# Optimization experiments

Hardware: AMD Instinct MI355X
Metric: run time of the kernel (lower is better)

The kernel has to match this reference:

```python
import jax, jax.numpy as jnp
import numpy as np

NUM_USERS = 50000
NUM_MOVIES = 20000
NNZ = 2000000
NUM_POS = NNZ // 10
NEG_SAMPLE_SIZE = 5
IN_FEATS = 128
NUM_HIDDEN = 64
BETA = 0.01
GAMMA = 0.01


def setup_inputs() -> dict:
    key = jax.random.key(0)
    ks = jax.random.split(key, 10)
    features = jax.random.normal(ks[0], (NUM_MOVIES, IN_FEATS), dtype=jnp.float32)
    W_enc = jax.random.normal(ks[1], (IN_FEATS, NUM_HIDDEN), dtype=jnp.float32) / np.sqrt(IN_FEATS)
    b_enc = jnp.zeros((NUM_HIDDEN,), dtype=jnp.float32)
    W_p = jax.random.normal(ks[2], (NUM_HIDDEN, NUM_HIDDEN), dtype=jnp.float32) / np.sqrt(NUM_HIDDEN)
    W_q = jax.random.normal(ks[3], (NUM_HIDDEN, NUM_HIDDEN), dtype=jnp.float32) / np.sqrt(NUM_HIDDEN)
    b_u = jnp.zeros((NUM_USERS,), dtype=jnp.float32)
    b_i = jnp.zeros((NUM_MOVIES,), dtype=jnp.float32)
    vals = jax.random.uniform(ks[4], (NNZ,), dtype=jnp.float32) + 0.5  # positive ratings
    rows = jax.random.randint(ks[5], (NNZ,), 0, NUM_USERS, dtype=jnp.int32)
    cols = jax.random.randint(ks[6], (NNZ,), 0, NUM_MOVIES, dtype=jnp.int32)
    pos_idx = jax.random.randint(ks[7], (NUM_POS,), 0, NNZ, dtype=jnp.int32)
    neg_item_idx = jax.random.randint(ks[8], (NUM_POS * NEG_SAMPLE_SIZE,), 0, NUM_MOVIES, dtype=jnp.int32)
    return {
        "features": features, "W_enc": W_enc, "b_enc": b_enc,
        "W_p": W_p, "W_q": W_q, "b_u": b_u, "b_i": b_i,
        "vals": vals, "rows": rows, "cols": cols,
        "pos_idx": pos_idx, "neg_item_idx": neg_item_idx,
        "neg_sample_size": NEG_SAMPLE_SIZE,
    }


def reference(features, W_enc, b_enc, W_p, W_q, b_u, b_i,
              vals, rows, cols, pos_idx, neg_item_idx, neg_sample_size):
    # encode + gconv projections -> item factor matrices P, Q  [M, d]
    h = features @ W_enc + b_enc
    P = h @ W_p
    Q = h @ W_q

    # sparse COO matmul: user_emb_full[u] = sum_{(u,i) in spm} vals * P[i]
    user_emb_full = jax.ops.segment_sum(vals[:, None] * P[cols], rows,
                                        num_segments=NUM_USERS)  # [U, d]
    # user_deg = spm.dot(ones)
    user_deg = jax.ops.segment_sum(vals, rows, num_segments=NUM_USERS)  # [U]

    def est_rating(user_idx, item_idx):
        bu = b_u[user_idx]
        bi = b_i[item_idx]
        ue = user_emb_full[user_idx] / user_deg[user_idx][:, None]
        return bu + bi + jnp.sum(ue * Q[item_idx], axis=1)

    user_idx = rows[pos_idx]
    item_idx = cols[pos_idx]
    r_ui = est_rating(user_idx, item_idx)[:, None]                 # [P, 1]
    neg_user_idx = jnp.repeat(user_idx, neg_sample_size)
    neg_r_ui = est_rating(neg_user_idx, neg_item_idx).reshape(-1, neg_sample_size)  # [P, S]

    diff = 1.0 - (r_ui - neg_r_ui)
    loss = (jnp.sum(diff * diff) * 0.5
            + BETA * 0.5 * jnp.sum(P * P + Q * Q)
            + GAMMA * 0.5 * (jnp.sum(b_u * b_u) + jnp.sum(b_i * b_i)))
    return loss
```

## Files before the change

### kernel.cpp

```cpp
#include <hip/hip_runtime.h>

#define HIDDEN 64
#define BETA 0.01f
#define GAMMA 0.01f

#define BUCKET_SHIFT 8
#define BUCKET_W     (1 << BUCKET_SHIFT)
#define TILE_E       8192

__device__ inline unsigned short f2bf(float f) {
    unsigned x = __float_as_uint(f);
    return (unsigned short)((x + 0x7fffu + ((x >> 16) & 1u)) >> 16);
}
__device__ inline float bf2f(unsigned short b) {
    return __uint_as_float(((unsigned)b) << 16);
}
__device__ inline float bflo(unsigned w) { return __uint_as_float(w << 16); }
__device__ inline float bfhi(unsigned w) {
    return __uint_as_float(w & 0xffff0000u);
}

__global__ void __launch_bounds__(256)
encode_kernel(const float* __restrict__ features,
              const float* __restrict__ W_enc,
              const float* __restrict__ b_enc,
              const float* __restrict__ W_p,
              const float* __restrict__ W_q,
              unsigned short* __restrict__ Ph,
              unsigned short* __restrict__ Qh,
              float* __restrict__ partials, int slot_base,
              int num_movies, int in_feats) {
    __shared__ float hs[16][HIDDEN];
    const int tid = threadIdx.x;
    const int j = tid & 63;
    const int wv = tid >> 6;
    const int m0 = blockIdx.x * 16 + wv * 4;

    const int c0 = min(m0 + 0, num_movies - 1);
    const int c1 = min(m0 + 1, num_movies - 1);
    const int c2 = min(m0 + 2, num_movies - 1);
    const int c3 = min(m0 + 3, num_movies - 1);
    const float* fr0 = features + (size_t)c0 * in_feats;
    const float* fr1 = features + (size_t)c1 * in_feats;
    const float* fr2 = features + (size_t)c2 * in_feats;
    const float* fr3 = features + (size_t)c3 * in_feats;

    float h0 = 0.0f, h1 = 0.0f, h2 = 0.0f, h3 = 0.0f;
    #pragma unroll 4
    for (int f = 0; f < in_feats; f += 4) {
        const float w_a = W_enc[(f + 0) * HIDDEN + j];
        const float w_b = W_enc[(f + 1) * HIDDEN + j];
        const float w_c = W_enc[(f + 2) * HIDDEN + j];
        const float w_d = W_enc[(f + 3) * HIDDEN + j];
        const float4 a0 = *(const float4*)(fr0 + f);
        const float4 a1 = *(const float4*)(fr1 + f);
        const float4 a2 = *(const float4*)(fr2 + f);
        const float4 a3 = *(const float4*)(fr3 + f);
        h0 = fmaf(a0.x, w_a, h0); h0 = fmaf(a0.y, w_b, h0);
        h0 = fmaf(a0.z, w_c, h0); h0 = fmaf(a0.w, w_d, h0);
        h1 = fmaf(a1.x, w_a, h1); h1 = fmaf(a1.y, w_b, h1);
        h1 = fmaf(a1.z, w_c, h1); h1 = fmaf(a1.w, w_d, h1);
        h2 = fmaf(a2.x, w_a, h2); h2 = fmaf(a2.y, w_b, h2);
        h2 = fmaf(a2.z, w_c, h2); h2 = fmaf(a2.w, w_d, h2);
        h3 = fmaf(a3.x, w_a, h3); h3 = fmaf(a3.y, w_b, h3);
        h3 = fmaf(a3.z, w_c, h3); h3 = fmaf(a3.w, w_d, h3);
    }
    const float be = b_enc[j];
    hs[wv * 4 + 0][j] = h0 + be;
    hs[wv * 4 + 1][j] = h1 + be;
    hs[wv * 4 + 2][j] = h2 + be;
    hs[wv * 4 + 3][j] = h3 + be;
    __syncthreads();

    float p0 = 0.0f, p1 = 0.0f, p2 = 0.0f, p3 = 0.0f;
    float q0 = 0.0f, q1 = 0.0f, q2 = 0.0f, q3 = 0.0f;
    #pragma unroll 4
    for (int f = 0; f < HIDDEN; f += 4) {
        const float wp0 = W_p[(f + 0) * HIDDEN + j];
        const float wp1 = W_p[(f + 1) * HIDDEN + j];
        const float wp2 = W_p[(f + 2) * HIDDEN + j];
        const float wp3 = W_p[(f + 3) * HIDDEN + j];
        const float wq0 = W_q[(f + 0) * HIDDEN + j];
        const float wq1 = W_q[(f + 1) * HIDDEN + j];
        const float wq2 = W_q[(f + 2) * HIDDEN + j];
        const float wq3 = W_q[(f + 3) * HIDDEN + j];
        const float4 v0 = *(const float4*)(&hs[wv * 4 + 0][f]);
        const float4 v1 = *(const float4*)(&hs[wv * 4 + 1][f]);
        const float4 v2 = *(const float4*)(&hs[wv * 4 + 2][f]);
        const float4 v3 = *(const float4*)(&hs[wv * 4 + 3][f]);
        p0 = fmaf(v0.x, wp0, p0); p0 = fmaf(v0.y, wp1, p0);
        p0 = fmaf(v0.z, wp2, p0); p0 = fmaf(v0.w, wp3, p0);
        q0 = fmaf(v0.x, wq0, q0); q0 = fmaf(v0.y, wq1, q0);
        q0 = fmaf(v0.z, wq2, q0); q0 = fmaf(v0.w, wq3, q0);
        p1 = fmaf(v1.x, wp0, p1); p1 = fmaf(v1.y, wp1, p1);
        p1 = fmaf(v1.z, wp2, p1); p1 = fmaf(v1.w, wp3, p1);
        q1 = fmaf(v1.x, wq0, q1); q1 = fmaf(v1.y, wq1, q1);
        q1 = fmaf(v1.z, wq2, q1); q1 = fmaf(v1.w, wq3, q1);
        p2 = fmaf(v2.x, wp0, p2); p2 = fmaf(v2.y, wp1, p2);
        p2 = fmaf(v2.z, wp2, p2); p2 = fmaf(v2.w, wp3, p2);
        q2 = fmaf(v2.x, wq0, q2); q2 = fmaf(v2.y, wq1, q2);
        q2 = fmaf(v2.z, wq2, q2); q2 = fmaf(v2.w, wq3, q2);
        p3 = fmaf(v3.x, wp0, p3); p3 = fmaf(v3.y, wp1, p3);
        p3 = fmaf(v3.z, wp2, p3); p3 = fmaf(v3.w, wp3, p3);
        q3 = fmaf(v3.x, wq0, q3); q3 = fmaf(v3.y, wq1, q3);
        q3 = fmaf(v3.z, wq2, q3); q3 = fmaf(v3.w, wq3, q3);
    }

    float reg = 0.0f;
    if (m0 + 0 < num_movies) {
        Ph[(size_t)(m0 + 0) * HIDDEN + j] = f2bf(p0);
        Qh[(size_t)(m0 + 0) * HIDDEN + j] = f2bf(q0);
        reg += p0 * p0 + q0 * q0;
    }
    if (m0 + 1 < num_movies) {
        Ph[(size_t)(m0 + 1) * HIDDEN + j] = f2bf(p1);
        Qh[(size_t)(m0 + 1) * HIDDEN + j] = f2bf(q1);
        reg += p1 * p1 + q1 * q1;
    }
    if (m0 + 2 < num_movies) {
        Ph[(size_t)(m0 + 2) * HIDDEN + j] = f2bf(p2);
        Qh[(size_t)(m0 + 2) * HIDDEN + j] = f2bf(q2);
        reg += p2 * p2 + q2 * q2;
    }
    if (m0 + 3 < num_movies) {
        Ph[(size_t)(m0 + 3) * HIDDEN + j] = f2bf(p3);
        Qh[(size_t)(m0 + 3) * HIDDEN + j] = f2bf(q3);
        reg += p3 * p3 + q3 * q3;
    }

    for (int off = 32; off; off >>= 1) reg += __shfl_down(reg, off);
    __shared__ float s_part[4];
    if (j == 0) s_part[wv] = reg;
    __syncthreads();
    if (tid == 0) {
        float t = (s_part[0] + s_part[1]) + (s_part[2] + s_part[3]);
        partials[slot_base + blockIdx.x] = 0.5f * BETA * t;
    }
}

__global__ void tilehist_kernel(const int* __restrict__ rows, int nnz,
                                int nbuckets, int ntiles,
                                unsigned* __restrict__ tileHist) {
    extern __shared__ unsigned hist[];
    const int t = blockIdx.x;
    const int tid = threadIdx.x;
    for (int i = tid; i < nbuckets; i += blockDim.x) hist[i] = 0;
    __syncthreads();

    const int base = t * TILE_E;
    const int kmax = TILE_E / 256;
    for (int k = 0; k < kmax; ++k) {
        const int e = base + k * 256 + tid;
        if (e < nnz) {
            const int r = __builtin_nontemporal_load(rows + e);
            atomicAdd(&hist[r >> BUCKET_SHIFT], 1u);
        }
    }
    __syncthreads();
    for (int i = tid; i < nbuckets; i += blockDim.x)
        tileHist[(size_t)i * ntiles + t] = hist[i];
}

__global__ void chunksum_kernel(const unsigned* __restrict__ src, int n,
                                unsigned* __restrict__ sums) {
    __shared__ unsigned s[256];
    const int t = threadIdx.x;
    const int i = blockIdx.x * 256 + t;
    s[t] = (i < n) ? src[i] : 0u;
    __syncthreads();
    for (int off = 128; off; off >>= 1) {
        if (t < off) s[t] += s[t + off];
        __syncthreads();
    }
    if (t == 0) sums[blockIdx.x] = s[0];
}

__global__ void __launch_bounds__(512)
scantop_kernel(const unsigned* __restrict__ sums, int nchunks,
               unsigned* __restrict__ chunk_off,
               unsigned* __restrict__ offs, int n, int total) {
    __shared__ unsigned s[512];
    const int t = threadIdx.x;
    unsigned x = (t < nchunks) ? sums[t] : 0u;
    s[t] = x;
    __syncthreads();
    for (int off = 1; off < 512; off <<= 1) {
        unsigned v = (t >= off) ? s[t - off] : 0u;
        __syncthreads();
        s[t] += v;
        __syncthreads();
    }
    if (t < nchunks) chunk_off[t] = s[t] - x;
    if (t == 0) offs[n] = (unsigned)total;
}

__global__ void exscan_kernel(const unsigned* __restrict__ src, int n,
                              const unsigned* __restrict__ chunk_off,
                              unsigned* __restrict__ dst) {
    __shared__ unsigned s[256];
    const int t = threadIdx.x;
    const int i = blockIdx.x * 256 + t;
    unsigned x = (i < n) ? src[i] : 0u;
    s[t] = x;
    __syncthreads();
    for (int off = 1; off < 256; off <<= 1) {
        unsigned v = (t >= off) ? s[t - off] : 0u;
        __syncthreads();
        s[t] += v;
        __syncthreads();
    }
    if (i < n) dst[i] = chunk_off[blockIdx.x] + s[t] - x;
}

__global__ void partition_kernel(const int* __restrict__ rows,
                                 const int* __restrict__ cols,
                                 const float* __restrict__ vals, int nnz,
                                 int nbuckets, int ntiles,
                                 const unsigned* __restrict__ offsB,
                                 uint2* __restrict__ temp) {
    extern __shared__ unsigned smem[];
    unsigned* hist = smem;
    unsigned* lofs = smem + nbuckets;
    const int t = blockIdx.x;
    const int tid = threadIdx.x;
    for (int i = tid; i < nbuckets; i += blockDim.x) {
        hist[i] = 0;
        lofs[i] = offsB[(size_t)i * ntiles + t];
    }
    __syncthreads();

    const int base = t * TILE_E;
    const int kmax = TILE_E / 256;
    for (int k = 0; k < kmax; ++k) {
        const int e = base + k * 256 + tid;
        if (e < nnz) {
            const int r = __builtin_nontemporal_load(rows + e);
            const int c = __builtin_nontemporal_load(cols + e);
            const float v = __builtin_nontemporal_load(vals + e);
            const int b = r >> BUCKET_SHIFT;
            const unsigned lrank = atomicAdd(&hist[b], 1u);
            const unsigned dst = lofs[b] + lrank;
            const unsigned key = ((unsigned)r << 15) | (unsigned)c;
            temp[dst] = make_uint2(key, __float_as_uint(v));
        }
    }
}

__global__ void __launch_bounds__(1024)
csr_scatter_kernel(const uint2* __restrict__ temp,
                   const unsigned* __restrict__ offsB,
                   int* __restrict__ row_start,
                   uint2* __restrict__ pairs,
                   int ntiles, int num_users, int nbB) {
    __shared__ int cnt[BUCKET_W];
    __shared__ int scan_s[BUCKET_W];
    __shared__ int cur[BUCKET_W];
    const int b = blockIdx.x;
    const int tid = threadIdx.x;
    const int ubase = b << BUCKET_SHIFT;
    const int s0 = (int)offsB[(size_t)b * ntiles];
    const int s1 = (int)offsB[(size_t)(b + 1) * ntiles];

    if (tid < BUCKET_W) cnt[tid] = 0;
    __syncthreads();
    const unsigned* tx = (const unsigned*)temp;
    for (int s = s0 + tid; s < s1; s += 1024) {
        const unsigned key = __builtin_nontemporal_load(tx + 2 * (size_t)s);
        atomicAdd(&cnt[(int)(key >> 15) - ubase], 1);
    }
    __syncthreads();

    int x = 0;
    if (tid < BUCKET_W) {
        x = cnt[tid];
        scan_s[tid] = x;
    }
    __syncthreads();
    for (int off = 1; off < BUCKET_W; off <<= 1) {
        int v = 0;
        if (tid < BUCKET_W && tid >= off) v = scan_s[tid - off];
        __syncthreads();
        if (tid < BUCKET_W) scan_s[tid] += v;
        __syncthreads();
    }
    if (tid < BUCKET_W) {
        const int start = s0 + scan_s[tid] - x;
        cur[tid] = start;
        if (ubase + tid < num_users) row_start[ubase + tid] = start;
    }
    if (b == nbB - 1 && tid == 0) row_start[num_users] = s1;
    __syncthreads();

    for (int s = s0 + tid; s < s1; s += 1024) {
        const unsigned long long ev = __builtin_nontemporal_load(
            (const unsigned long long*)temp + s);
        const unsigned ex = (unsigned)ev;
        const unsigned ey = (unsigned)(ev >> 32);
        const int lu = (int)(ex >> 15) - ubase;
        const int dst = atomicAdd(&cur[lu], 1);
        pairs[dst] = make_uint2(ex & 0x7fffu, ey);
    }
}

__global__ void gather_kernel(const int* __restrict__ row_start,
                              const uint2* __restrict__ pairs,
                              const unsigned short* __restrict__ Ph,
                              float* __restrict__ user_emb,
                              float* __restrict__ user_deg, int nu) {
    const int lane = threadIdx.x & 63;
    const int q  = lane >> 4;
    const int ql = lane & 15;
    const int u = (blockIdx.x * blockDim.x + threadIdx.x) >> 6;
    if (u >= nu) return;

    const int s0 = row_start[u];
    const int s1 = row_start[u + 1];
    float a0 = 0.0f, a1 = 0.0f, a2 = 0.0f, a3 = 0.0f, degA = 0.0f;
    float b0 = 0.0f, b1 = 0.0f, b2 = 0.0f, b3 = 0.0f, degB = 0.0f;
    int s = s0;
    for (; s + 7 < s1; s += 8) {
        const uint2 pA = pairs[s + q];
        const uint2 pB = pairs[s + 4 + q];
        const uint2 wA = *(const uint2*)(Ph + (size_t)pA.x * HIDDEN + 4 * ql);
        const uint2 wB = *(const uint2*)(Ph + (size_t)pB.x * HIDDEN + 4 * ql);
        const float vA = __uint_as_float(pA.y);
        const float vB = __uint_as_float(pB.y);
        a0 = fmaf(vA, bflo(wA.x), a0);
        a1 = fmaf(vA, bfhi(wA.x), a1);
        a2 = fmaf(vA, bflo(wA.y), a2);
        a3 = fmaf(vA, bfhi(wA.y), a3);
        b0 = fmaf(vB, bflo(wB.x), b0);
        b1 = fmaf(vB, bfhi(wB.x), b1);
        b2 = fmaf(vB, bflo(wB.y), b2);
        b3 = fmaf(vB, bfhi(wB.y), b3);
        degA += vA;
        degB += vB;
    }
    for (; s + 3 < s1; s += 4) {
        const uint2 pA = pairs[s + q];
        const uint2 wA = *(const uint2*)(Ph + (size_t)pA.x * HIDDEN + 4 * ql);
        const float vA = __uint_as_float(pA.y);
        a0 = fmaf(vA, bflo(wA.x), a0);
        a1 = fmaf(vA, bfhi(wA.x), a1);
        a2 = fmaf(vA, bflo(wA.y), a2);
        a3 = fmaf(vA, bfhi(wA.y), a3);
        degA += vA;
    }
    if (s + q < s1) {
        const uint2 pA = pairs[s + q];
        const uint2 wA = *(const uint2*)(Ph + (size_t)pA.x * HIDDEN + 4 * ql);
        const float vA = __uint_as_float(pA.y);
        a0 = fmaf(vA, bflo(wA.x), a0);
        a1 = fmaf(vA, bfhi(wA.x), a1);
        a2 = fmaf(vA, bflo(wA.y), a2);
        a3 = fmaf(vA, bfhi(wA.y), a3);
        degA += vA;
    }

    float x0 = a0 + b0, x1 = a1 + b1, x2 = a2 + b2, x3 = a3 + b3;
    float deg = degA + degB;
    x0 += __shfl_xor(x0, 16); x0 += __shfl_xor(x0, 32);
    x1 += __shfl_xor(x1, 16); x1 += __shfl_xor(x1, 32);
    x2 += __shfl_xor(x2, 16); x2 += __shfl_xor(x2, 32);
    x3 += __shfl_xor(x3, 16); x3 += __shfl_xor(x3, 32);
    deg += __shfl_xor(deg, 16); deg += __shfl_xor(deg, 32);
    if (q == 0) {
        *(float4*)(user_emb + (size_t)u * HIDDEN + 4 * ql) =
            make_float4(x0, x1, x2, x3);
        if (ql == 0) user_deg[u] = deg;
    }
}

__device__ inline float dot16(const uint4* __restrict__ q,
                              const float* __restrict__ ue) {
    float d = 0.0f;
    #pragma unroll
    for (int h = 0; h < 2; ++h) {
        const uint4 v = q[h];
        const unsigned w0 = v.x, w1 = v.y, w2 = v.z, w3 = v.w;
        d = fmaf(ue[h * 8 + 0], bflo(w0), d);
        d = fmaf(ue[h * 8 + 1], bfhi(w0), d);
        d = fmaf(ue[h * 8 + 2], bflo(w1), d);
        d = fmaf(ue[h * 8 + 3], bfhi(w1), d);
        d = fmaf(ue[h * 8 + 4], bflo(w2), d);
        d = fmaf(ue[h * 8 + 5], bfhi(w2), d);
        d = fmaf(ue[h * 8 + 6], bflo(w3), d);
        d = fmaf(ue[h * 8 + 7], bfhi(w3), d);
    }
    return d;
}

template <int S>
__global__ void loss4_kernel(const float* __restrict__ user_emb,
                             const float* __restrict__ user_deg,
                             const unsigned short* __restrict__ Qh,
                             const float* __restrict__ b_u,
                             const float* __restrict__ b_i,
                             const int* __restrict__ rows,
                             const int* __restrict__ cols,
                             const int* __restrict__ pos_idx,
                             const int* __restrict__ neg_item_idx,
                             int num_pos,
                             float* __restrict__ partials, int slot_base) {
    const int tid = blockIdx.x * blockDim.x + threadIdx.x;
    const int g = tid >> 2;
    const int l = tid & 3;
    float acc = 0.0f;

    if (g < num_pos) {
        const int e = pos_idx[g];
        const int u = rows[e];
        const int ii = cols[e];
        const float invdeg = 1.0f / user_deg[u];

        float ue[16];
        {
            const float4* uep =
                (const float4*)(user_emb + (size_t)u * HIDDEN + l * 16);
            #pragma unroll
            for (int k = 0; k < 4; ++k) {
                const float4 t4 = uep[k];
                ue[4 * k + 0] = t4.x * invdeg;
                ue[4 * k + 1] = t4.y * invdeg;
                ue[4 * k + 2] = t4.z * invdeg;
                ue[4 * k + 3] = t4.w * invdeg;
            }
        }

        int jarr[S];
        float part[1 + S];
        part[0] = dot16((const uint4*)(Qh + (size_t)ii * HIDDEN + l * 16), ue);
        #pragma unroll
        for (int s = 0; s < S; ++s) {
            const int j = neg_item_idx[(size_t)g * S + s];
            jarr[s] = j;
            part[1 + s] =
                dot16((const uint4*)(Qh + (size_t)j * HIDDEN + l * 16), ue);
        }

        #pragma unroll
        for (int k = 0; k < 1 + S; ++k) {
            part[k] += __shfl_xor(part[k], 1);
            part[k] += __shfl_xor(part[k], 2);
        }

        if (l == 0) {
            const float bu = b_u[u];
            const float r = bu + b_i[ii] + part[0];
            #pragma unroll
            for (int s = 0; s < S; ++s) {
                const float nr = bu + b_i[jarr[s]] + part[1 + s];
                const float diff = 1.0f - (r - nr);
                acc += 0.5f * diff * diff;
            }
        }
    }

    for (int off = 32; off; off >>= 1) acc += __shfl_down(acc, off);
    __shared__ float s_part[16];
    const int wave = threadIdx.x >> 6;
    const int lane = threadIdx.x & 63;
    if (lane == 0) s_part[wave] = acc;
    __syncthreads();
    if (threadIdx.x == 0) {
        float t = 0.0f;
        const int nw = blockDim.x >> 6;
        for (int w = 0; w < nw; ++w) t += s_part[w];
        partials[slot_base + blockIdx.x] = t;
    }
}

__global__ void loss_generic_kernel(const float* __restrict__ user_emb,
                                    const float* __restrict__ user_deg,
                                    const unsigned short* __restrict__ Qh,
                                    const float* __restrict__ b_u,
                                    const float* __restrict__ b_i,
                                    const int* __restrict__ rows,
                                    const int* __restrict__ cols,
                                    const int* __restrict__ pos_idx,
                                    const int* __restrict__ neg_item_idx,
                                    int num_pos, int S,
                                    float* __restrict__ partials,
                                    int slot_base) {
    const int p = blockIdx.x * blockDim.x + threadIdx.x;
    float acc = 0.0f;
    if (p < num_pos) {
        const int e = pos_idx[p];
        const int u = rows[e];
        const int ii = cols[e];
        const float invdeg = 1.0f / user_deg[u];
        float ue[HIDDEN];
        #pragma unroll
        for (int kk = 0; kk < HIDDEN; ++kk)
            ue[kk] = user_emb[(size_t)u * HIDDEN + kk] * invdeg;
        const float bu = b_u[u];
        float dot = 0.0f;
        #pragma unroll
        for (int kk = 0; kk < HIDDEN; ++kk)
            dot = fmaf(ue[kk], bf2f(Qh[(size_t)ii * HIDDEN + kk]), dot);
        const float rr = bu + b_i[ii] + dot;
        for (int s = 0; s < S; ++s) {
            const int j = neg_item_idx[(size_t)p * S + s];
            float dn = 0.0f;
            #pragma unroll
            for (int kk = 0; kk < HIDDEN; ++kk)
                dn = fmaf(ue[kk], bf2f(Qh[(size_t)j * HIDDEN + kk]), dn);
            const float nr = bu + b_i[j] + dn;
            const float diff = 1.0f - (rr - nr);
            acc += 0.5f * diff * diff;
        }
    }
    for (int off = 32; off; off >>= 1) acc += __shfl_down(acc, off);
    __shared__ float s_part[16];
    const int wave = threadIdx.x >> 6;
    const int lane = threadIdx.x & 63;
    if (lane == 0) s_part[wave] = acc;
    __syncthreads();
    if (threadIdx.x == 0) {
        float t = 0.0f;
        const int nw = blockDim.x >> 6;
        for (int w = 0; w < nw; ++w) t += s_part[w];
        partials[slot_base + blockIdx.x] = t;
    }
}

__global__ void __launch_bounds__(1024)
final_reduce_kernel(const float* __restrict__ partials, int n,
                    const float* __restrict__ b_u, int nu,
                    const float* __restrict__ b_i, int ni,
                    float* __restrict__ out) {
    __shared__ float s[1024];
    const int t = threadIdx.x;
    float a = 0.0f;
    for (int i = t; i < n; i += 1024) a += partials[i];
    float r = 0.0f;
    for (int i = t; i < nu; i += 1024) {
        const float v = b_u[i];
        r = fmaf(v, v, r);
    }
    for (int i = t; i < ni; i += 1024) {
        const float v = b_i[i];
        r = fmaf(v, v, r);
    }
    s[t] = a + 0.5f * GAMMA * r;
    __syncthreads();
    for (int off = 512; off; off >>= 1) {
        if (t < off) s[t] += s[t + off];
        __syncthreads();
    }
    if (t == 0) out[0] = s[0];
}

extern "C" void kernel_launch(void* const* d_in, const int* in_sizes, int n_in,
                              void* d_out, int out_size, void* d_ws, size_t ws_size,
                              hipStream_t stream) {
    const float* features     = (const float*)d_in[0];
    const float* W_enc        = (const float*)d_in[1];
    const float* b_enc        = (const float*)d_in[2];
    const float* W_p          = (const float*)d_in[3];
    const float* W_q          = (const float*)d_in[4];
    const float* b_u          = (const float*)d_in[5];
    const float* b_i          = (const float*)d_in[6];
    const float* vals         = (const float*)d_in[7];
    const int*   rows         = (const int*)d_in[8];
    const int*   cols         = (const int*)d_in[9];
    const int*   pos_idx      = (const int*)d_in[10];
    const int*   neg_item_idx = (const int*)d_in[11];

    const int num_users  = in_sizes[5];
    const int num_movies = in_sizes[6];
    const int in_feats   = in_sizes[0] / num_movies;
    const int nnz        = in_sizes[7];
    const int num_pos    = in_sizes[10];
    const int S          = in_sizes[11] / num_pos;

    const int nbB    = (num_users + BUCKET_W - 1) >> BUCKET_SHIFT;
    const int ntiles = (nnz + TILE_E - 1) / TILE_E;
    const int scanNB = nbB * ntiles;
    const int n1b    = (scanNB + 255) / 256;

    const int enc_blocks  = (num_movies + 15) / 16;
    const int loss_blocks = (S == 5) ? (int)(((size_t)num_pos * 4 + 255) / 256)
                                     : (num_pos + 255) / 256;
    const int slot_pq   = 0;
    const int slot_loss = enc_blocks;
    const int n_slots   = enc_blocks + loss_blocks;

    auto align256 = [](size_t x) { return (x + 255) & ~(size_t)255; };
    char* ws = (char*)d_ws;
    size_t off = 0;
    unsigned short* Ph = (unsigned short*)(ws + off);
    off += align256((size_t)num_movies * HIDDEN * 2);
    unsigned short* Qh = (unsigned short*)(ws + off);
    off += align256((size_t)num_movies * HIDDEN * 2);
    char* U = ws + off;
    const size_t emb_bytes = align256((size_t)num_users * HIDDEN * 4);
    const size_t tmp_bytes = align256((size_t)nnz * 8);
    uint2* temp     = (uint2*)U;
    float* user_emb = (float*)U;
    off += (emb_bytes > tmp_bytes) ? emb_bytes : tmp_bytes;
    float* user_deg = (float*)(ws + off); off += align256((size_t)num_users * 4);
    int*   row_start= (int*)(ws + off);   off += align256((size_t)(num_users + 1) * 4);
    unsigned* tileHistB = (unsigned*)(ws + off); off += align256((size_t)scanNB * 4);
    unsigned* offsB     = (unsigned*)(ws + off); off += align256((size_t)(scanNB + 1) * 4);
    unsigned* sums_b    = (unsigned*)(ws + off); off += align256(512 * 4);
    unsigned* top_b     = (unsigned*)(ws + off); off += align256(512 * 4);
    uint2* pairs        = (uint2*)(ws + off);    off += align256((size_t)nnz * 8);
    float* partials     = (float*)(ws + off);    off += align256((size_t)n_slots * 4);

    float* out = (float*)d_out;

    encode_kernel<<<enc_blocks, 256, 0, stream>>>(
        features, W_enc, b_enc, W_p, W_q, Ph, Qh, partials, slot_pq,
        num_movies, in_feats);

    tilehist_kernel<<<ntiles, 256, (size_t)nbB * 4, stream>>>(
        rows, nnz, nbB, ntiles, tileHistB);
    chunksum_kernel<<<n1b, 256, 0, stream>>>(tileHistB, scanNB, sums_b);
    scantop_kernel<<<1, 512, 0, stream>>>(sums_b, n1b, top_b, offsB, scanNB, nnz);
    exscan_kernel<<<n1b, 256, 0, stream>>>(tileHistB, scanNB, top_b, offsB);

    partition_kernel<<<ntiles, 256, (size_t)nbB * 8, stream>>>(
        rows, cols, vals, nnz, nbB, ntiles, offsB, temp);
    csr_scatter_kernel<<<nbB, 1024, 0, stream>>>(temp, offsB, row_start,
                                                 pairs, ntiles, num_users, nbB);

    gather_kernel<<<(num_users * 64 + 255) / 256, 256, 0, stream>>>(
        row_start, pairs, Ph, user_emb, user_deg, num_users);

    if (S == 5) {
        loss4_kernel<5><<<loss_blocks, 256, 0, stream>>>(
            user_emb, user_deg, Qh, b_u, b_i, rows, cols, pos_idx,
            neg_item_idx, num_pos, partials, slot_loss);
    } else {
        loss_generic_kernel<<<loss_blocks, 256, 0, stream>>>(
            user_emb, user_deg, Qh, b_u, b_i, rows, cols, pos_idx,
            neg_item_idx, num_pos, S, partials, slot_loss);
    }

    final_reduce_kernel<<<1, 1024, 0, stream>>>(partials, n_slots,
                                                b_u, num_users,
                                                b_i, num_movies, out);
}
```

Measured before the change: 180.7 us.

## Compute per-user row offsets via global histogram scan; prefetch pairs in gather

Per-user counts are now accumulated with global atomics during the tile histogram pass, then scanned with the existing chunksum/scantop/exscan kernels to produce row_start. This removes the in-bucket count pass and shared-memory scan from csr_scatter. The gather loop is software-pipelined so the next pair loads are issued before the current Ph loads, and index loads use nontemporal hints. In exchange it adds 2M global atomics on a 50K-entry array, a memset, and three extra small kernel launches.

```diff
diff --git a/kernel.cpp b/kernel.cpp
--- a/kernel.cpp
+++ b/kernel.cpp
@@ -140,7 +140,8 @@
 
 __global__ void tilehist_kernel(const int* __restrict__ rows, int nnz,
                                 int nbuckets, int ntiles,
-                                unsigned* __restrict__ tileHist) {
+                                unsigned* __restrict__ tileHist,
+                                int* __restrict__ counts_u) {
     extern __shared__ unsigned hist[];
     const int t = blockIdx.x;
     const int tid = threadIdx.x;
@@ -154,6 +155,7 @@
         if (e < nnz) {
             const int r = __builtin_nontemporal_load(rows + e);
             atomicAdd(&hist[r >> BUCKET_SHIFT], 1u);
+            atomicAdd(&counts_u[r], 1);
         }
     }
     __syncthreads();
@@ -249,11 +251,9 @@
 __global__ void __launch_bounds__(1024)
 csr_scatter_kernel(const uint2* __restrict__ temp,
                    const unsigned* __restrict__ offsB,
-                   int* __restrict__ row_start,
+                   const int* __restrict__ row_start,
                    uint2* __restrict__ pairs,
-                   int ntiles, int num_users, int nbB) {
-    __shared__ int cnt[BUCKET_W];
-    __shared__ int scan_s[BUCKET_W];
+                   int ntiles, int num_users) {
     __shared__ int cur[BUCKET_W];
     const int b = blockIdx.x;
     const int tid = threadIdx.x;
@@ -261,34 +261,10 @@
     const int s0 = (int)offsB[(size_t)b * ntiles];
     const int s1 = (int)offsB[(size_t)(b + 1) * ntiles];
 
-    if (tid < BUCKET_W) cnt[tid] = 0;
-    __syncthreads();
-    const unsigned* tx = (const unsigned*)temp;
-    for (int s = s0 + tid; s < s1; s += 1024) {
-        const unsigned key = __builtin_nontemporal_load(tx + 2 * (size_t)s);
-        atomicAdd(&cnt[(int)(key >> 15) - ubase], 1);
-    }
-    __syncthreads();
-
-    int x = 0;
     if (tid < BUCKET_W) {
-        x = cnt[tid];
-        scan_s[tid] = x;
-    }
-    __syncthreads();
-    for (int off = 1; off < BUCKET_W; off <<= 1) {
-        int v = 0;
-        if (tid < BUCKET_W && tid >= off) v = scan_s[tid - off];
-        __syncthreads();
-        if (tid < BUCKET_W) scan_s[tid] += v;
-        __syncthreads();
-    }
-    if (tid < BUCKET_W) {
-        const int start = s0 + scan_s[tid] - x;
-        cur[tid] = start;
-        if (ubase + tid < num_users) row_start[ubase + tid] = start;
-    }
-    if (b == nbB - 1 && tid == 0) row_start[num_users] = s1;
+        const int gu = ubase + tid;
+        cur[tid] = (gu < num_users) ? row_start[gu] : 0;
+    }
     __syncthreads();
 
     for (int s = s0 + tid; s < s1; s += 1024) {
@@ -300,6 +276,12 @@
         const int dst = atomicAdd(&cur[lu], 1);
         pairs[dst] = make_uint2(ex & 0x7fffu, ey);
     }
+}
+
+__device__ inline uint2 ldnt2(const uint2* p) {
+    const unsigned long long v =
+        __builtin_nontemporal_load((const unsigned long long*)p);
+    return make_uint2((unsigned)v, (unsigned)(v >> 32));
 }
 
 __global__ void gather_kernel(const int* __restrict__ row_start,
@@ -317,27 +299,54 @@
     const int s1 = row_start[u + 1];
     float a0 = 0.0f, a1 = 0.0f, a2 = 0.0f, a3 = 0.0f, degA = 0.0f;
     float b0 = 0.0f, b1 = 0.0f, b2 = 0.0f, b3 = 0.0f, degB = 0.0f;
+
+    const int n8 = (s1 - s0) >> 3;
     int s = s0;
-    for (; s + 7 < s1; s += 8) {
-        const uint2 pA = pairs[s + q];
-        const uint2 pB = pairs[s + 4 + q];
-        const uint2 wA = *(const uint2*)(Ph + (size_t)pA.x * HIDDEN + 4 * ql);
-        const uint2 wB = *(const uint2*)(Ph + (size_t)pB.x * HIDDEN + 4 * ql);
-        const float vA = __uint_as_float(pA.y);
-        const float vB = __uint_as_float(pB.y);
-        a0 = fmaf(vA, bflo(wA.x), a0);
-        a1 = fmaf(vA, bfhi(wA.x), a1);
-        a2 = fmaf(vA, bflo(wA.y), a2);
-        a3 = fmaf(vA, bfhi(wA.y), a3);
-        b0 = fmaf(vB, bflo(wB.x), b0);
-        b1 = fmaf(vB, bfhi(wB.x), b1);
-        b2 = fmaf(vB, bflo(wB.y), b2);
-        b3 = fmaf(vB, bfhi(wB.y), b3);
-        degA += vA;
-        degB += vB;
-    }
-    for (; s + 3 < s1; s += 4) {
-        const uint2 pA = pairs[s + q];
+    if (n8 > 0) {
+        uint2 pA = ldnt2(pairs + s + q);
+        uint2 pB = ldnt2(pairs + s + 4 + q);
+        for (int it = 1; it < n8; ++it) {
+            const int sn = s + 8;
+            const uint2 nA = ldnt2(pairs + sn + q);
+            const uint2 nB = ldnt2(pairs + sn + 4 + q);
+            const uint2 wA = *(const uint2*)(Ph + (size_t)pA.x * HIDDEN + 4 * ql);
+            const uint2 wB = *(const uint2*)(Ph + (size_t)pB.x * HIDDEN + 4 * ql);
+            const float vA = __uint_as_float(pA.y);
+            const float vB = __uint_as_float(pB.y);
+            a0 = fmaf(vA, bflo(wA.x), a0);
+            a1 = fmaf(vA, bfhi(wA.x), a1);
+            a2 = fmaf(vA, bflo(wA.y), a2);
+            a3 = fmaf(vA, bfhi(wA.y), a3);
+            b0 = fmaf(vB, bflo(wB.x), b0);
+            b1 = fmaf(vB, bfhi(wB.x), b1);
+            b2 = fmaf(vB, bflo(wB.y), b2);
+            b3 = fmaf(vB, bfhi(wB.y), b3);
+            degA += vA;
+            degB += vB;
+            pA = nA;
+            pB = nB;
+            s = sn;
+        }
+        {
+            const uint2 wA = *(const uint2*)(Ph + (size_t)pA.x * HIDDEN + 4 * ql);
+            const uint2 wB = *(const uint2*)(Ph + (size_t)pB.x * HIDDEN + 4 * ql);
+            const float vA = __uint_as_float(pA.y);
+            const float vB = __uint_as_float(pB.y);
+            a0 = fmaf(vA, bflo(wA.x), a0);
+            a1 = fmaf(vA, bfhi(wA.x), a1);
+            a2 = fmaf(vA, bflo(wA.y), a2);
+            a3 = fmaf(vA, bfhi(wA.y), a3);
+            b0 = fmaf(vB, bflo(wB.x), b0);
+            b1 = fmaf(vB, bfhi(wB.x), b1);
+            b2 = fmaf(vB, bflo(wB.y), b2);
+            b3 = fmaf(vB, bfhi(wB.y), b3);
+            degA += vA;
+            degB += vB;
+            s += 8;
+        }
+    }
+    if (s + 3 < s1) {
+        const uint2 pA = ldnt2(pairs + s + q);
         const uint2 wA = *(const uint2*)(Ph + (size_t)pA.x * HIDDEN + 4 * ql);
         const float vA = __uint_as_float(pA.y);
         a0 = fmaf(vA, bflo(wA.x), a0);
@@ -345,9 +354,10 @@
         a2 = fmaf(vA, bflo(wA.y), a2);
         a3 = fmaf(vA, bfhi(wA.y), a3);
         degA += vA;
+        s += 4;
     }
     if (s + q < s1) {
-        const uint2 pA = pairs[s + q];
+        const uint2 pA = ldnt2(pairs + s + q);
         const uint2 wA = *(const uint2*)(Ph + (size_t)pA.x * HIDDEN + 4 * ql);
         const float vA = __uint_as_float(pA.y);
         a0 = fmaf(vA, bflo(wA.x), a0);
@@ -408,7 +418,7 @@
     float acc = 0.0f;
 
     if (g < num_pos) {
-        const int e = pos_idx[g];
+        const int e = __builtin_nontemporal_load(pos_idx + g);
         const int u = rows[e];
         const int ii = cols[e];
         const float invdeg = 1.0f / user_deg[u];
@@ -432,7 +442,8 @@
         part[0] = dot16((const uint4*)(Qh + (size_t)ii * HIDDEN + l * 16), ue);
         #pragma unroll
         for (int s = 0; s < S; ++s) {
-            const int j = neg_item_idx[(size_t)g * S + s];
+            const int j = __builtin_nontemporal_load(
+                neg_item_idx + (size_t)g * S + s);
             jarr[s] = j;
             part[1 + s] =
                 dot16((const uint4*)(Qh + (size_t)j * HIDDEN + l * 16), ue);
@@ -578,6 +589,7 @@
     const int ntiles = (nnz + TILE_E - 1) / TILE_E;
     const int scanNB = nbB * ntiles;
     const int n1b    = (scanNB + 255) / 256;
+    const int n1u    = (num_users + 255) / 256;
 
     const int enc_blocks  = (num_movies + 15) / 16;
     const int loss_blocks = (S == 5) ? (int)(((size_t)num_pos * 4 + 255) / 256)
@@ -600,30 +612,42 @@
     float* user_emb = (float*)U;
     off += (emb_bytes > tmp_bytes) ? emb_bytes : tmp_bytes;
     float* user_deg = (float*)(ws + off); off += align256((size_t)num_users * 4);
+    int*   counts_u = (int*)(ws + off);   off += align256((size_t)num_users * 4);
     int*   row_start= (int*)(ws + off);   off += align256((size_t)(num_users + 1) * 4);
     unsigned* tileHistB = (unsigned*)(ws + off); off += align256((size_t)scanNB * 4);
     unsigned* offsB     = (unsigned*)(ws + off); off += align256((size_t)(scanNB + 1) * 4);
     unsigned* sums_b    = (unsigned*)(ws + off); off += align256(512 * 4);
     unsigned* top_b     = (unsigned*)(ws + off); off += align256(512 * 4);
+    unsigned* sums_u    = (unsigned*)(ws + off); off += align256(512 * 4);
+    unsigned* top_u     = (unsigned*)(ws + off); off += align256(512 * 4);
     uint2* pairs        = (uint2*)(ws + off);    off += align256((size_t)nnz * 8);
     float* partials     = (float*)(ws + off);    off += align256((size_t)n_slots * 4);
 
     float* out = (float*)d_out;
+
+    hipMemsetAsync(counts_u, 0, (size_t)num_users * 4, stream);
 
     encode_kernel<<<enc_blocks, 256, 0, stream>>>(
         features, W_enc, b_enc, W_p, W_q, Ph, Qh, partials, slot_pq,
         num_movies, in_feats);
 
     tilehist_kernel<<<ntiles, 256, (size_t)nbB * 4, stream>>>(
-        rows, nnz, nbB, ntiles, tileHistB);
+        rows, nnz, nbB, ntiles, tileHistB, counts_u);
     chunksum_kernel<<<n1b, 256, 0, stream>>>(tileHistB, scanNB, sums_b);
     scantop_kernel<<<1, 512, 0, stream>>>(sums_b, n1b, top_b, offsB, scanNB, nnz);
     exscan_kernel<<<n1b, 256, 0, stream>>>(tileHistB, scanNB, top_b, offsB);
 
+    chunksum_kernel<<<n1u, 256, 0, stream>>>((const unsigned*)counts_u,
+                                             num_users, sums_u);
+    scantop_kernel<<<1, 512, 0, stream>>>(sums_u, n1u, top_u,
+                                          (unsigned*)row_start, num_users, nnz);
+    exscan_kernel<<<n1u, 256, 0, stream>>>((const unsigned*)counts_u, num_users,
+                                           top_u, (unsigned*)row_start);
+
     partition_kernel<<<ntiles, 256, (size_t)nbB * 8, stream>>>(
         rows, cols, vals, nnz, nbB, ntiles, offsB, temp);
     csr_scatter_kernel<<<nbB, 1024, 0, stream>>>(temp, offsB, row_start,
-                                                 pairs, ntiles, num_users, nbB);
+                                                 pairs, ntiles, num_users);
 
     gather_kernel<<<(num_users * 64 + 255) / 256, 256, 0, stream>>>(
         row_start, pairs, Ph, user_emb, user_deg, num_users);
```

Result: slower. 266.9 us (+47.7%).

## Fuse CSR scatter and gather into one kernel using LDS-sorted buckets

Applied to the files above, without the earlier changes.

Merges the per-bucket CSR scatter and the per-user gather into a single kernel. Each 128-user bucket sorts its edges by user in shared memory (in chunks of up to 6144 edges) and then gathers and accumulates P rows straight from that buffer, so the global pairs array and row_start are no longer written and read back. It halves the bucket width so each block does less work, and handles overflow chunks with a read-modify-write into user_emb. The cost is fewer, larger blocks whose gather phase runs only 8 waves per block, which may expose more memory latency than the old one-wave-per-user launch.

```diff
diff --git a/kernel.cpp b/kernel.cpp
--- a/kernel.cpp
+++ b/kernel.cpp
@@ -4,9 +4,10 @@
 #define BETA 0.01f
 #define GAMMA 0.01f
 
-#define BUCKET_SHIFT 8
+#define BUCKET_SHIFT 7
 #define BUCKET_W     (1 << BUCKET_SHIFT)
 #define TILE_E       8192
+#define CAP          6144
 
 __device__ inline unsigned short f2bf(float f) {
     unsigned x = __float_as_uint(f);
@@ -246,129 +247,142 @@
     }
 }
 
-__global__ void __launch_bounds__(1024)
-csr_scatter_kernel(const uint2* __restrict__ temp,
-                   const unsigned* __restrict__ offsB,
-                   int* __restrict__ row_start,
-                   uint2* __restrict__ pairs,
-                   int ntiles, int num_users, int nbB) {
+__global__ void __launch_bounds__(512)
+scatter_gather_kernel(const uint2* __restrict__ temp,
+                      const unsigned* __restrict__ offsB,
+                      const unsigned short* __restrict__ Ph,
+                      float* __restrict__ user_emb,
+                      float* __restrict__ user_deg,
+                      int ntiles, int num_users) {
+    __shared__ uint2 ebuf[CAP];
     __shared__ int cnt[BUCKET_W];
-    __shared__ int scan_s[BUCKET_W];
+    __shared__ int lstart[BUCKET_W];
     __shared__ int cur[BUCKET_W];
+
     const int b = blockIdx.x;
     const int tid = threadIdx.x;
     const int ubase = b << BUCKET_SHIFT;
     const int s0 = (int)offsB[(size_t)b * ntiles];
     const int s1 = (int)offsB[(size_t)(b + 1) * ntiles];
 
-    if (tid < BUCKET_W) cnt[tid] = 0;
-    __syncthreads();
-    const unsigned* tx = (const unsigned*)temp;
-    for (int s = s0 + tid; s < s1; s += 1024) {
-        const unsigned key = __builtin_nontemporal_load(tx + 2 * (size_t)s);
-        atomicAdd(&cnt[(int)(key >> 15) - ubase], 1);
-    }
-    __syncthreads();
-
-    int x = 0;
-    if (tid < BUCKET_W) {
-        x = cnt[tid];
-        scan_s[tid] = x;
-    }
-    __syncthreads();
-    for (int off = 1; off < BUCKET_W; off <<= 1) {
-        int v = 0;
-        if (tid < BUCKET_W && tid >= off) v = scan_s[tid - off];
-        __syncthreads();
-        if (tid < BUCKET_W) scan_s[tid] += v;
-        __syncthreads();
-    }
-    if (tid < BUCKET_W) {
-        const int start = s0 + scan_s[tid] - x;
-        cur[tid] = start;
-        if (ubase + tid < num_users) row_start[ubase + tid] = start;
-    }
-    if (b == nbB - 1 && tid == 0) row_start[num_users] = s1;
-    __syncthreads();
-
-    for (int s = s0 + tid; s < s1; s += 1024) {
-        const unsigned long long ev = __builtin_nontemporal_load(
-            (const unsigned long long*)temp + s);
-        const unsigned ex = (unsigned)ev;
-        const unsigned ey = (unsigned)(ev >> 32);
-        const int lu = (int)(ex >> 15) - ubase;
-        const int dst = atomicAdd(&cur[lu], 1);
-        pairs[dst] = make_uint2(ex & 0x7fffu, ey);
-    }
-}
-
-__global__ void gather_kernel(const int* __restrict__ row_start,
-                              const uint2* __restrict__ pairs,
-                              const unsigned short* __restrict__ Ph,
-                              float* __restrict__ user_emb,
-                              float* __restrict__ user_deg, int nu) {
-    const int lane = threadIdx.x & 63;
-    const int q  = lane >> 4;
+    const int wv = tid >> 6;
+    const int lane = tid & 63;
+    const int q = lane >> 4;
     const int ql = lane & 15;
-    const int u = (blockIdx.x * blockDim.x + threadIdx.x) >> 6;
-    if (u >= nu) return;
-
-    const int s0 = row_start[u];
-    const int s1 = row_start[u + 1];
-    float a0 = 0.0f, a1 = 0.0f, a2 = 0.0f, a3 = 0.0f, degA = 0.0f;
-    float b0 = 0.0f, b1 = 0.0f, b2 = 0.0f, b3 = 0.0f, degB = 0.0f;
-    int s = s0;
-    for (; s + 7 < s1; s += 8) {
-        const uint2 pA = pairs[s + q];
-        const uint2 pB = pairs[s + 4 + q];
-        const uint2 wA = *(const uint2*)(Ph + (size_t)pA.x * HIDDEN + 4 * ql);
-        const uint2 wB = *(const uint2*)(Ph + (size_t)pB.x * HIDDEN + 4 * ql);
-        const float vA = __uint_as_float(pA.y);
-        const float vB = __uint_as_float(pB.y);
-        a0 = fmaf(vA, bflo(wA.x), a0);
-        a1 = fmaf(vA, bfhi(wA.x), a1);
-        a2 = fmaf(vA, bflo(wA.y), a2);
-        a3 = fmaf(vA, bfhi(wA.y), a3);
-        b0 = fmaf(vB, bflo(wB.x), b0);
-        b1 = fmaf(vB, bfhi(wB.x), b1);
-        b2 = fmaf(vB, bflo(wB.y), b2);
-        b3 = fmaf(vB, bfhi(wB.y), b3);
-        degA += vA;
-        degB += vB;
-    }
-    for (; s + 3 < s1; s += 4) {
-        const uint2 pA = pairs[s + q];
-        const uint2 wA = *(const uint2*)(Ph + (size_t)pA.x * HIDDEN + 4 * ql);
-        const float vA = __uint_as_float(pA.y);
-        a0 = fmaf(vA, bflo(wA.x), a0);
-        a1 = fmaf(vA, bfhi(wA.x), a1);
-        a2 = fmaf(vA, bflo(wA.y), a2);
-        a3 = fmaf(vA, bfhi(wA.y), a3);
-        degA += vA;
-    }
-    if (s + q < s1) {
-        const uint2 pA = pairs[s + q];
-        const uint2 wA = *(const uint2*)(Ph + (size_t)pA.x * HIDDEN + 4 * ql);
-        const float vA = __uint_as_float(pA.y);
-        a0 = fmaf(vA, bflo(wA.x), a0);
-        a1 = fmaf(vA, bfhi(wA.x), a1);
-        a2 = fmaf(vA, bflo(wA.y), a2);
-        a3 = fmaf(vA, bfhi(wA.y), a3);
-        degA += vA;
-    }
-
-    float x0 = a0 + b0, x1 = a1 + b1, x2 = a2 + b2, x3 = a3 + b3;
-    float deg = degA + degB;
-    x0 += __shfl_xor(x0, 16); x0 += __shfl_xor(x0, 32);
-    x1 += __shfl_xor(x1, 16); x1 += __shfl_xor(x1, 32);
-    x2 += __shfl_xor(x2, 16); x2 += __shfl_xor(x2, 32);
-    x3 += __shfl_xor(x3, 16); x3 += __shfl_xor(x3, 32);
-    deg += __shfl_xor(deg, 16); deg += __shfl_xor(deg, 32);
-    if (q == 0) {
-        *(float4*)(user_emb + (size_t)u * HIDDEN + 4 * ql) =
-            make_float4(x0, x1, x2, x3);
-        if (ql == 0) user_deg[u] = deg;
-    }
+
+    bool first = true;
+    int cbase = s0;
+    do {
+        const int cend = min(cbase + CAP, s1);
+
+        if (tid < BUCKET_W) cnt[tid] = 0;
+        __syncthreads();
+        for (int s = cbase + tid; s < cend; s += 512)
+            atomicAdd(&cnt[(int)(temp[s].x >> 15) - ubase], 1);
+        __syncthreads();
+
+        int x = 0;
+        if (tid < BUCKET_W) { x = cnt[tid]; lstart[tid] = x; }
+        __syncthreads();
+        for (int off = 1; off < BUCKET_W; off <<= 1) {
+            int v = 0;
+            if (tid < BUCKET_W && tid >= off) v = lstart[tid - off];
+            __syncthreads();
+            if (tid < BUCKET_W) lstart[tid] += v;
+            __syncthreads();
+        }
+        if (tid < BUCKET_W) {
+            const int st = lstart[tid] - x;
+            lstart[tid] = st;
+            cur[tid] = st;
+        }
+        __syncthreads();
+
+        for (int s = cbase + tid; s < cend; s += 512) {
+            const uint2 e = temp[s];
+            const int lu = (int)(e.x >> 15) - ubase;
+            const int pos = atomicAdd(&cur[lu], 1);
+            ebuf[pos] = make_uint2(e.x & 0x7fffu, e.y);
+        }
+        __syncthreads();
+
+        for (int k = 0; k < 16; ++k) {
+            const int lu = wv * 16 + k;
+            const int gu = ubase + lu;
+            if (gu >= num_users) break;
+            const int ls = lstart[lu];
+            const int le = cur[lu];
+            float a0 = 0.0f, a1 = 0.0f, a2 = 0.0f, a3 = 0.0f, dA = 0.0f;
+            float c0 = 0.0f, c1 = 0.0f, c2 = 0.0f, c3 = 0.0f, dB = 0.0f;
+            int i = ls;
+            for (; i + 7 < le; i += 8) {
+                const uint2 eA = ebuf[i + q];
+                const uint2 eB = ebuf[i + 4 + q];
+                const uint2 wA =
+                    *(const uint2*)(Ph + (size_t)eA.x * HIDDEN + 4 * ql);
+                const uint2 wB =
+                    *(const uint2*)(Ph + (size_t)eB.x * HIDDEN + 4 * ql);
+                const float vA = __uint_as_float(eA.y);
+                const float vB = __uint_as_float(eB.y);
+                a0 = fmaf(vA, bflo(wA.x), a0);
+                a1 = fmaf(vA, bfhi(wA.x), a1);
+                a2 = fmaf(vA, bflo(wA.y), a2);
+                a3 = fmaf(vA, bfhi(wA.y), a3);
+                c0 = fmaf(vB, bflo(wB.x), c0);
+                c1 = fmaf(vB, bfhi(wB.x), c1);
+                c2 = fmaf(vB, bflo(wB.y), c2);
+                c3 = fmaf(vB, bfhi(wB.y), c3);
+                dA += vA;
+                dB += vB;
+            }
+            for (; i + 3 < le; i += 4) {
+                const uint2 eA = ebuf[i + q];
+                const uint2 wA =
+                    *(const uint2*)(Ph + (size_t)eA.x * HIDDEN + 4 * ql);
+                const float vA = __uint_as_float(eA.y);
+                a0 = fmaf(vA, bflo(wA.x), a0);
+                a1 = fmaf(vA, bfhi(wA.x), a1);
+                a2 = fmaf(vA, bflo(wA.y), a2);
+                a3 = fmaf(vA, bfhi(wA.y), a3);
+                dA += vA;
+            }
+            if (i + q < le) {
+                const uint2 eA = ebuf[i + q];
+                const uint2 wA =
+                    *(const uint2*)(Ph + (size_t)eA.x * HIDDEN + 4 * ql);
+                const float vA = __uint_as_float(eA.y);
+                a0 = fmaf(vA, bflo(wA.x), a0);
+                a1 = fmaf(vA, bfhi(wA.x), a1);
+                a2 = fmaf(vA, bflo(wA.y), a2);
+                a3 = fmaf(vA, bfhi(wA.y), a3);
+                dA += vA;
+            }
+
+            float x0 = a0 + c0, x1 = a1 + c1, x2 = a2 + c2, x3 = a3 + c3;
+            float deg = dA + dB;
+            x0 += __shfl_xor(x0, 16); x0 += __shfl_xor(x0, 32);
+            x1 += __shfl_xor(x1, 16); x1 += __shfl_xor(x1, 32);
+            x2 += __shfl_xor(x2, 16); x2 += __shfl_xor(x2, 32);
+            x3 += __shfl_xor(x3, 16); x3 += __shfl_xor(x3, 32);
+            deg += __shfl_xor(deg, 16); deg += __shfl_xor(deg, 32);
+            if (q == 0) {
+                float4* dst = (float4*)(user_emb + (size_t)gu * HIDDEN + 4 * ql);
+                if (first) {
+                    *dst = make_float4(x0, x1, x2, x3);
+                } else {
+                    const float4 o = *dst;
+                    *dst = make_float4(o.x + x0, o.y + x1, o.z + x2, o.w + x3);
+                }
+                if (ql == 0) {
+                    if (first) user_deg[gu] = deg;
+                    else user_deg[gu] += deg;
+                }
+            }
+        }
+        __syncthreads();
+        first = false;
+        cbase += CAP;
+    } while (cbase < s1);
 }
 
 __device__ inline float dot16(const uint4* __restrict__ q,
@@ -593,19 +607,13 @@
     off += align256((size_t)num_movies * HIDDEN * 2);
     unsigned short* Qh = (unsigned short*)(ws + off);
     off += align256((size_t)num_movies * HIDDEN * 2);
-    char* U = ws + off;
-    const size_t emb_bytes = align256((size_t)num_users * HIDDEN * 4);
-    const size_t tmp_bytes = align256((size_t)nnz * 8);
-    uint2* temp     = (uint2*)U;
-    float* user_emb = (float*)U;
-    off += (emb_bytes > tmp_bytes) ? emb_bytes : tmp_bytes;
+    uint2* temp     = (uint2*)(ws + off); off += align256((size_t)nnz * 8);
+    float* user_emb = (float*)(ws + off); off += align256((size_t)num_users * HIDDEN * 4);
     float* user_deg = (float*)(ws + off); off += align256((size_t)num_users * 4);
-    int*   row_start= (int*)(ws + off);   off += align256((size_t)(num_users + 1) * 4);
     unsigned* tileHistB = (unsigned*)(ws + off); off += align256((size_t)scanNB * 4);
     unsigned* offsB     = (unsigned*)(ws + off); off += align256((size_t)(scanNB + 1) * 4);
     unsigned* sums_b    = (unsigned*)(ws + off); off += align256(512 * 4);
     unsigned* top_b     = (unsigned*)(ws + off); off += align256(512 * 4);
-    uint2* pairs        = (uint2*)(ws + off);    off += align256((size_t)nnz * 8);
     float* partials     = (float*)(ws + off);    off += align256((size_t)n_slots * 4);
 
     float* out = (float*)d_out;
@@ -622,11 +630,9 @@
 
     partition_kernel<<<ntiles, 256, (size_t)nbB * 8, stream>>>(
         rows, cols, vals, nnz, nbB, ntiles, offsB, temp);
-    csr_scatter_kernel<<<nbB, 1024, 0, stream>>>(temp, offsB, row_start,
-                                                 pairs, ntiles, num_users, nbB);
-
-    gather_kernel<<<(num_users * 64 + 255) / 256, 256, 0, stream>>>(
-        row_start, pairs, Ph, user_emb, user_deg, num_users);
+
+    scatter_gather_kernel<<<nbB, 512, 0, stream>>>(
+        temp, offsB, Ph, user_emb, user_deg, ntiles, num_users);
 
     if (S == 5) {
         loss4_kernel<5><<<loss_blocks, 256, 0, stream>>>(
```

Result: faster. 167.2 us (-7.5%).
